# Kernel optimization log

Hardware: AMD Instinct MI355X
Metric: run time of the kernel (lower is better)

The kernel has to match this reference:

```python
import jax, jax.numpy as jnp
import numpy as np

L, N, H = 32768, 256, 256


def _binop(ei, ej):
    a_i, bu_i = ei
    a_j, bu_j = ej
    return (a_j * a_i, a_j * bu_i + bu_j)


def setup_inputs() -> dict:
    key = jax.random.key(0)
    ks = jax.random.split(key, 9)
    # Param values follow init_lru_parameters statistics for numerical sanity.
    u1 = jax.random.uniform(ks[0], (N,), minval=1e-3, maxval=1.0)
    u2 = jax.random.uniform(ks[1], (N,), minval=1e-3, maxval=1.0)
    nu_log = jnp.log(-0.5 * jnp.log(u1))
    theta_log = jnp.log(6.28 * u2)
    B_re = jax.random.normal(ks[2], (N, H)) / np.sqrt(2.0 * H)
    B_im = jax.random.normal(ks[3], (N, H)) / np.sqrt(2.0 * H)
    C_re = jax.random.normal(ks[4], (H, N)) / np.sqrt(1.0 * N)
    C_im = jax.random.normal(ks[5], (H, N)) / np.sqrt(1.0 * N)
    D = jax.random.normal(ks[6], (H,))
    diag_lambda = jnp.exp(-jnp.exp(nu_log) + 1j * jnp.exp(theta_log))
    gamma_log = jnp.log(jnp.sqrt(1.0 - jnp.abs(diag_lambda) ** 2))
    x = jax.random.normal(ks[7], (L, H), dtype=jnp.float32)
    f32 = lambda a: a.astype(jnp.float32)
    return {"x": x, "nu_log": f32(nu_log), "theta_log": f32(theta_log),
            "B_re": f32(B_re), "B_im": f32(B_im), "C_re": f32(C_re),
            "C_im": f32(C_im), "D": f32(D), "gamma_log": f32(gamma_log)}


def reference(x, nu_log, theta_log, B_re, B_im, C_re, C_im, D, gamma_log):
    # Diagonal complex LRU: x_t = Lambda * x_{t-1} + B_norm u_t ; y_t = Re(C x_t) + D*u_t
    Lambda = jnp.exp(-jnp.exp(nu_log) + 1j * jnp.exp(theta_log))        # (N,) complex
    B_norm = (B_re + 1j * B_im) * jnp.exp(gamma_log)[:, None]           # (N,H)
    C = C_re + 1j * C_im                                                # (H,N)
    Bu = x.astype(B_norm.dtype) @ B_norm.T                              # (L,N) complex
    Lam_el = jnp.broadcast_to(Lambda[None, :], Bu.shape)                # (L,N)
    _, states = jax.lax.associative_scan(_binop, (Lam_el, Bu))          # (L,N) complex
    y = (states @ C.T).real + x * D                                     # (L,H) real
    return y
```

## Files before the change

### kernel.cpp

```cpp
#include <hip/hip_runtime.h>

#define L_SEQ 32768
#define NDIM 256
#define HDIM 256
#define NCAT 512
#define LC 64
#define NCHUNK 512

typedef unsigned short u16;
typedef unsigned int u32;
typedef __bf16 bf16x8 __attribute__((ext_vector_type(8)));
typedef float f32x4 __attribute__((ext_vector_type(4)));
typedef __attribute__((address_space(3))) void lds_void;
typedef const __attribute__((address_space(1))) void gbl_void;

__device__ __forceinline__ u16 f2bf(float f) {
  u32 u = __builtin_bit_cast(u32, f);
  u = u + 0x7fffu + ((u >> 16) & 1u);
  return (u16)(u >> 16);
}
__device__ __forceinline__ float bf2f(u16 v) {
  u32 u = ((u32)v) << 16;
  return __builtin_bit_cast(float, u);
}

__global__ __launch_bounds__(256) void prep_kernel(
    const float* __restrict__ x,
    const float* __restrict__ nu_log, const float* __restrict__ theta_log,
    const float* __restrict__ B_re, const float* __restrict__ B_im,
    const float* __restrict__ C_re, const float* __restrict__ C_im,
    const float* __restrict__ gamma_log,
    u16* __restrict__ x_bf, u16* __restrict__ Bcat, u16* __restrict__ Ccat,
    float2* __restrict__ lam, float2* __restrict__ lam64)
{
  const int blk = blockIdx.x, tid = threadIdx.x;
  if (blk < 2048) {
    const float4* src = ((const float4*)x) + (size_t)blk * 1024;
    ushort4* dst = ((ushort4*)x_bf) + (size_t)blk * 1024;
#pragma unroll
    for (int j = 0; j < 4; ++j) {
      float4 v = src[j * 256 + tid];
      dst[j * 256 + tid] = make_ushort4(f2bf(v.x), f2bf(v.y), f2bf(v.z), f2bf(v.w));
    }
  } else if (blk < 2560) {
    int b2 = blk - 2048;
    int jj = b2 >> 1, p = b2 & 1;
    float g = expf(gamma_log[jj]);
    const float* src = (p ? B_im : B_re) + (size_t)jj * HDIM;
    Bcat[(size_t)b2 * HDIM + tid] = f2bf(src[tid] * g);
  } else if (blk < 2816) {
    int h = blk - 2560;
#pragma unroll
    for (int half = 0; half < 2; ++half) {
      int nc = half * 256 + tid;
      int jj = nc >> 1, p = nc & 1;
      float v = p ? -C_im[(size_t)h * NDIM + jj] : C_re[(size_t)h * NDIM + jj];
      Ccat[(size_t)h * NCAT + nc] = f2bf(v);
    }
  } else {
    float nu_e = expf(nu_log[tid]);
    float th = expf(theta_log[tid]);
    float r = expf(-nu_e);
    lam[tid] = make_float2(r * cosf(th), r * sinf(th));
    float r64 = expf(-(float)LC * nu_e);
    float ph = (float)LC * th;
    lam64[tid] = make_float2(r64 * cosf(ph), r64 * sinf(ph));
  }
}

__global__ __launch_bounds__(256) void gemm1_kernel(
    const u16* __restrict__ A,
    const u16* __restrict__ Bm,
    u16* __restrict__ Cout,
    int M, int N, int K)
{
  constexpr int BM = 128, BN = 128, BK = 32;
  __shared__ u16 lA[BM * BK];
  __shared__ u16 lB[BN * BK];
  const int tid = threadIdx.x;
  const int lane = tid & 63, wave = tid >> 6;
  const int bn = blockIdx.x, bm = blockIdx.y;
  const int row0 = bm * BM, col0 = bn * BN;
  const int wm = (wave >> 1) * 64, wn = (wave & 1) * 64;
  const int fr = lane & 15, fo = (lane >> 4) * 8;

  f32x4 acc[4][4] = {};
  const int nkt = K / BK;
  for (int kt = 0; kt < nkt; ++kt) {
    const int k0 = kt * BK;
#pragma unroll
    for (int j = 0; j < 2; ++j) {
      int chunk = j * 256 + tid;
      int r = chunk >> 2, c = chunk & 3;
      const u16* ga = A + (size_t)(row0 + r) * K + (k0 + c * 8);
      const u16* gb = Bm + (size_t)(col0 + r) * K + (k0 + c * 8);
      __builtin_amdgcn_global_load_lds((gbl_void*)ga, (lds_void*)&lA[chunk * 8], 16, 0, 0);
      __builtin_amdgcn_global_load_lds((gbl_void*)gb, (lds_void*)&lB[chunk * 8], 16, 0, 0);
    }
    __syncthreads();

    bf16x8 af[4], bfr[4];
#pragma unroll
    for (int i = 0; i < 4; ++i) {
      af[i]  = *reinterpret_cast<const bf16x8*>(&lA[(wm + i * 16 + fr) * BK + fo]);
      bfr[i] = *reinterpret_cast<const bf16x8*>(&lB[(wn + i * 16 + fr) * BK + fo]);
    }
#pragma unroll
    for (int i = 0; i < 4; ++i)
#pragma unroll
      for (int j = 0; j < 4; ++j)
        acc[i][j] = __builtin_amdgcn_mfma_f32_16x16x32_bf16(af[i], bfr[j], acc[i][j], 0, 0, 0);
    __syncthreads();
  }

  const int fq = lane >> 4;
#pragma unroll
  for (int i = 0; i < 4; ++i)
#pragma unroll
    for (int j = 0; j < 4; ++j) {
      int cg = col0 + wn + j * 16 + fr;
#pragma unroll
      for (int r = 0; r < 4; ++r) {
        int rg = row0 + wm + i * 16 + fq * 4 + r;
        Cout[(size_t)rg * N + cg] = f2bf(acc[i][j][r]);
      }
    }
}

__global__ __launch_bounds__(256) void scan_carry_kernel(
    const ushort2* __restrict__ Bu2, const float2* __restrict__ lam,
    float2* __restrict__ carry)
{
  const int n = threadIdx.x, b = blockIdx.x;
  const float2 la = lam[n];
  float sre = 0.f, sim = 0.f;
  const ushort2* p = Bu2 + (size_t)b * LC * NDIM + n;
#pragma unroll 8
  for (int j = 0; j < LC; ++j) {
    ushort2 bu = p[(size_t)j * NDIM];
    float bre = bf2f(bu.x), bim = bf2f(bu.y);
    float nre = la.x * sre - la.y * sim + bre;
    float nim = la.x * sim + la.y * sre + bim;
    sre = nre; sim = nim;
  }
  carry[(size_t)b * NDIM + n] = make_float2(sre, sim);
}

__global__ __launch_bounds__(512) void carry_scan_kernel(
    const float2* __restrict__ carry, const float2* __restrict__ lam64,
    float2* __restrict__ corr)
{
  __shared__ float4 e[NCHUNK];
  const int n = blockIdx.x;
  const int b = threadIdx.x;
  float2 a = lam64[n];
  float2 v = carry[(size_t)b * NDIM + n];
  e[b] = make_float4(a.x, a.y, v.x, v.y);
  __syncthreads();
#pragma unroll
  for (int d = 1; d < NCHUNK; d <<= 1) {
    float4 prev;
    if (b >= d) prev = e[b - d];
    __syncthreads();
    if (b >= d) {
      float2 ap = make_float2(prev.x, prev.y), vp = make_float2(prev.z, prev.w);
      float2 na, nv;
      na.x = a.x * ap.x - a.y * ap.y;
      na.y = a.x * ap.y + a.y * ap.x;
      nv.x = a.x * vp.x - a.y * vp.y + v.x;
      nv.y = a.x * vp.y + a.y * vp.x + v.y;
      a = na; v = nv;
      e[b] = make_float4(a.x, a.y, v.x, v.y);
    }
    __syncthreads();
  }
  if (b == 0) corr[n] = make_float2(0.f, 0.f);
  if (b < NCHUNK - 1) corr[(size_t)(b + 1) * NDIM + n] = v;
}

__global__ __launch_bounds__(256) void gemm2_kernel(
    const u16* __restrict__ Bu,
    const u16* __restrict__ Cc,
    const float2* __restrict__ lam,
    const float2* __restrict__ corr,
    const u16* __restrict__ xbf,
    const float* __restrict__ Dv,
    float* __restrict__ out)
{
  constexpr int BM = 64, BN = 128, BK = 32, K = NCAT;
  __shared__ u16 sT[BM * K];
  __shared__ u16 lB1[BN * BK];
  const int tid = threadIdx.x;
  const int lane = tid & 63, wave = tid >> 6;
  const int bn = blockIdx.x, bm = blockIdx.y;
  const int row0 = bm * BM, col0 = bn * BN;
  const int wm = (wave >> 1) * 32, wn = (wave & 1) * 64;
  const int fr = lane & 15, fq = lane >> 4;
  char* sb = (char*)sT;

#pragma unroll
  for (int j = 0; j < 16; ++j) {
    int q = j * 256 + tid;
    int row = q >> 6, off = q & 63;
    const u16* g = Bu + (size_t)(row0 + row) * NCAT + off * 8;
    __builtin_amdgcn_global_load_lds((gbl_void*)g, (lds_void*)&sT[q * 8], 16, 0, 0);
  }
  float2 la = lam[tid];
  float2 c0 = corr[(size_t)bm * NDIM + tid];
  __syncthreads();

  {
    float sre = c0.x, sim = c0.y;
    ushort2 buf[8], nbuf[8];
    const int lb = tid * 4;
#pragma unroll
    for (int s = 0; s < 8; ++s) buf[s] = *(const ushort2*)(sb + s * 1024 + lb);
#pragma unroll
    for (int b8 = 0; b8 < 8; ++b8) {
      if (b8 < 7) {
#pragma unroll
        for (int s = 0; s < 8; ++s)
          nbuf[s] = *(const ushort2*)(sb + (b8 * 8 + 8 + s) * 1024 + lb);
      }
#pragma unroll
      for (int s = 0; s < 8; ++s) {
        int row = b8 * 8 + s;
        float bre = bf2f(buf[s].x), bim = bf2f(buf[s].y);
        float nre = la.x * sre - la.y * sim + bre;
        float nim = la.x * sim + la.y * sre + bim;
        sre = nre; sim = nim;
        *(ushort2*)(sb + row * 1024 + (lb ^ ((row & 7) << 4))) =
            make_ushort2(f2bf(sre), f2bf(sim));
      }
#pragma unroll
      for (int s = 0; s < 8; ++s) buf[s] = nbuf[s];
    }
  }
  __syncthreads();

  f32x4 acc[2][4] = {};
#pragma unroll 1
  for (int kt = 0; kt < 16; ++kt) {
#pragma unroll
    for (int j = 0; j < 2; ++j) {
      int q = j * 256 + tid;
      int row = q >> 2, c = q & 3;
      const u16* g = Cc + (size_t)(col0 + row) * K + kt * BK + c * 8;
      __builtin_amdgcn_global_load_lds((gbl_void*)g, (lds_void*)&lB1[q * 8], 16, 0, 0);
    }
    __syncthreads();

    bf16x8 af[2], bfr[4];
#pragma unroll
    for (int i = 0; i < 2; ++i) {
      int row = wm + i * 16 + fr;
      int wb = kt * 64 + fq * 16;
      af[i] = *(const bf16x8*)(sb + row * 1024 + (wb ^ ((row & 7) << 4)));
    }
#pragma unroll
    for (int j = 0; j < 4; ++j)
      bfr[j] = *(const bf16x8*)(&lB1[(wn + j * 16 + fr) * BK + fq * 8]);
#pragma unroll
    for (int i = 0; i < 2; ++i)
#pragma unroll
      for (int j = 0; j < 4; ++j)
        acc[i][j] = __builtin_amdgcn_mfma_f32_16x16x32_bf16(af[i], bfr[j], acc[i][j], 0, 0, 0);
    __syncthreads();
  }

#pragma unroll
  for (int i = 0; i < 2; ++i)
#pragma unroll
    for (int j = 0; j < 4; ++j) {
      int cg = col0 + wn + j * 16 + fr;
      float dvc = Dv[cg];
#pragma unroll
      for (int r = 0; r < 4; ++r) {
        int rg = row0 + wm + i * 16 + fq * 4 + r;
        float v = acc[i][j][r] + bf2f(xbf[(size_t)rg * HDIM + cg]) * dvc;
        out[(size_t)rg * HDIM + cg] = v;
      }
    }
}

extern "C" void kernel_launch(void* const* d_in, const int* in_sizes, int n_in,
                              void* d_out, int out_size, void* d_ws, size_t ws_size,
                              hipStream_t stream)
{
  (void)in_sizes; (void)n_in; (void)out_size; (void)ws_size;
  const float* x         = (const float*)d_in[0];
  const float* nu_log    = (const float*)d_in[1];
  const float* theta_log = (const float*)d_in[2];
  const float* B_re      = (const float*)d_in[3];
  const float* B_im      = (const float*)d_in[4];
  const float* C_re      = (const float*)d_in[5];
  const float* C_im      = (const float*)d_in[6];
  const float* Dv        = (const float*)d_in[7];
  const float* gamma_log = (const float*)d_in[8];

  char* ws = (char*)d_ws;
  u16*    x_bf  = (u16*)ws;
  u16*    Bu_bf = (u16*)(ws + ((size_t)16 << 20));
  u16*    Bcat  = (u16*)(ws + ((size_t)48 << 20));
  u16*    Ccat  = (u16*)(ws + ((size_t)48 << 20) + 262144);
  float2* lam   = (float2*)(ws + ((size_t)48 << 20) + 524288);
  float2* lam64 = (float2*)(ws + ((size_t)48 << 20) + 524288 + 4096);
  float2* carry = (float2*)(ws + ((size_t)49 << 20));
  float2* corr  = (float2*)(ws + ((size_t)50 << 20));

  prep_kernel<<<2817, 256, 0, stream>>>(x, nu_log, theta_log, B_re, B_im,
                                        C_re, C_im, gamma_log,
                                        x_bf, Bcat, Ccat, lam, lam64);

  gemm1_kernel<<<dim3(NCAT / 128, L_SEQ / 128), 256, 0, stream>>>(
      x_bf, Bcat, Bu_bf, L_SEQ, NCAT, HDIM);

  scan_carry_kernel<<<NCHUNK, 256, 0, stream>>>((const ushort2*)Bu_bf, lam, carry);

  carry_scan_kernel<<<NDIM, 512, 0, stream>>>(carry, lam64, corr);

  gemm2_kernel<<<dim3(HDIM / 128, L_SEQ / 64), 256, 0, stream>>>(
      Bu_bf, Ccat, lam, corr, x_bf, Dv, (float*)d_out);
}
```

Baseline: 83.58 us.

## Widen gemm2 tile to full output width to avoid redundant chunk rescans

The gemm2 kernel now covers all 256 output columns per block with 512 threads (8 waves), instead of two 128-column blocks per row tile. Before, each row chunk's in-LDS scan fixup and Bu tile load ran twice, once per column block; now each runs once. The first C tile load is also issued before the scan so it overlaps with it. In exchange, half the threads sit idle during the serial scan phase, LDS per block grows, and there are half as many blocks, which may reduce occupancy.

Measured after the change: 73.66 us. 1.13x faster.

```diff
diff --git a/kernel.cpp b/kernel.cpp
--- a/kernel.cpp
+++ b/kernel.cpp
@@ -178,7 +178,7 @@
   if (b < NCHUNK - 1) corr[(size_t)(b + 1) * NDIM + n] = v;
 }
 
-__global__ __launch_bounds__(256) void gemm2_kernel(
+__global__ __launch_bounds__(512, 4) void gemm2_kernel(
     const u16* __restrict__ Bu,
     const u16* __restrict__ Cc,
     const float2* __restrict__ lam,
@@ -187,29 +187,39 @@
     const float* __restrict__ Dv,
     float* __restrict__ out)
 {
-  constexpr int BM = 64, BN = 128, BK = 32, K = NCAT;
+  constexpr int BM = 64, BN = 256, BK = 32, K = NCAT;
   __shared__ u16 sT[BM * K];
   __shared__ u16 lB1[BN * BK];
   const int tid = threadIdx.x;
   const int lane = tid & 63, wave = tid >> 6;
-  const int bn = blockIdx.x, bm = blockIdx.y;
-  const int row0 = bm * BM, col0 = bn * BN;
-  const int wm = (wave >> 1) * 32, wn = (wave & 1) * 64;
+  const int bm = blockIdx.x;
+  const int row0 = bm * BM;
+  const int wm = (wave >> 2) * 32, wn = (wave & 3) * 64;
   const int fr = lane & 15, fq = lane >> 4;
   char* sb = (char*)sT;
 
 #pragma unroll
-  for (int j = 0; j < 16; ++j) {
-    int q = j * 256 + tid;
+  for (int j = 0; j < 8; ++j) {
+    int q = j * 512 + tid;
     int row = q >> 6, off = q & 63;
     const u16* g = Bu + (size_t)(row0 + row) * NCAT + off * 8;
     __builtin_amdgcn_global_load_lds((gbl_void*)g, (lds_void*)&sT[q * 8], 16, 0, 0);
   }
-  float2 la = lam[tid];
-  float2 c0 = corr[(size_t)bm * NDIM + tid];
+#pragma unroll
+  for (int j = 0; j < 2; ++j) {
+    int q = j * 512 + tid;
+    int row = q >> 2, c = q & 3;
+    const u16* g = Cc + (size_t)row * K + c * 8;
+    __builtin_amdgcn_global_load_lds((gbl_void*)g, (lds_void*)&lB1[q * 8], 16, 0, 0);
+  }
+  float2 la = make_float2(0.f, 0.f), c0 = make_float2(0.f, 0.f);
+  if (tid < 256) {
+    la = lam[tid];
+    c0 = corr[(size_t)bm * NDIM + tid];
+  }
   __syncthreads();
 
-  {
+  if (tid < 256) {
     float sre = c0.x, sim = c0.y;
     ushort2 buf[8], nbuf[8];
     const int lb = tid * 4;
@@ -241,12 +251,14 @@
   f32x4 acc[2][4] = {};
 #pragma unroll 1
   for (int kt = 0; kt < 16; ++kt) {
-#pragma unroll
-    for (int j = 0; j < 2; ++j) {
-      int q = j * 256 + tid;
-      int row = q >> 2, c = q & 3;
-      const u16* g = Cc + (size_t)(col0 + row) * K + kt * BK + c * 8;
-      __builtin_amdgcn_global_load_lds((gbl_void*)g, (lds_void*)&lB1[q * 8], 16, 0, 0);
+    if (kt > 0) {
+#pragma unroll
+      for (int j = 0; j < 2; ++j) {
+        int q = j * 512 + tid;
+        int row = q >> 2, c = q & 3;
+        const u16* g = Cc + (size_t)row * K + kt * BK + c * 8;
+        __builtin_amdgcn_global_load_lds((gbl_void*)g, (lds_void*)&lB1[q * 8], 16, 0, 0);
+      }
     }
     __syncthreads();
 
@@ -272,7 +284,7 @@
   for (int i = 0; i < 2; ++i)
 #pragma unroll
     for (int j = 0; j < 4; ++j) {
-      int cg = col0 + wn + j * 16 + fr;
+      int cg = wn + j * 16 + fr;
       float dvc = Dv[cg];
 #pragma unroll
       for (int r = 0; r < 4; ++r) {
@@ -319,6 +331,6 @@
 
   carry_scan_kernel<<<NDIM, 512, 0, stream>>>(carry, lam64, corr);
 
-  gemm2_kernel<<<dim3(HDIM / 128, L_SEQ / 64), 256, 0, stream>>>(
+  gemm2_kernel<<<NCHUNK, 512, 0, stream>>>(
       Bu_bf, Ccat, lam, corr, x_bf, Dv, (float*)d_out);
 }
```
